# Performance work log

Measured on AMD Instinct MI355X. Metric: run time of the kernel, lower is better.

## Reference

```python
import jax, jax.numpy as jnp
import numpy as np
from jax import lax

B, EMB, CIN, COUT, K, H, W = 16, 768, 64, 64, 3, 112, 112
HID = EMB // 4  # reduction_ratio=4
TOTAL = COUT * CIN * K * K


def setup_inputs() -> dict:
    key = jax.random.key(0)
    k1, k2, k3, k4 = jax.random.split(key, 4)
    cls_token = jax.random.normal(k1, (B, 1, EMB), dtype=jnp.float32)
    features = jax.random.normal(k2, (B, CIN, H, W), dtype=jnp.float32)
    W1 = jax.random.normal(k3, (EMB, HID), dtype=jnp.float32) * 0.02
    b1 = jnp.zeros((HID,), dtype=jnp.float32)
    W2 = jax.random.normal(k4, (HID, TOTAL), dtype=jnp.float32) * 0.01
    b2 = jnp.zeros((TOTAL,), dtype=jnp.float32)
    return {"cls_token": cls_token, "features": features,
            "W1": W1, "b1": b1, "W2": W2, "b2": b2}


def _per_sample_conv(feat, kern):
    # feat: (CIN, H, W); kern: (COUT, CIN, K, K) -> (COUT, H, W)
    out = lax.conv_general_dilated(
        feat[None], kern, window_strides=(1, 1), padding="SAME",
        dimension_numbers=("NCHW", "OIHW", "NCHW"))
    return out[0]


def reference(cls_token, features, W1, b1, W2, b2):
    # Dynamic kernel generation from CLS token
    x = cls_token[:, 0, :]                      # (B, EMB)
    h = jax.nn.relu(x @ W1 + b1)                # (B, HID)
    params = jnp.tanh(h @ W2 + b2)              # (B, TOTAL)
    kernel = params.reshape(B, COUT, CIN, K, K)
    # Per-sample convolution (equivalent to unfold + bmm in torch)
    conv_feat = jax.vmap(_per_sample_conv)(features, kernel)  # (B, COUT, H, W)
    # in_channels == out_channels -> identity shortcut
    return conv_feat + features
```

## Files before the change

### kernel.cpp

```cpp
#include <hip/hip_runtime.h>
#include <hip/hip_bf16.h>

#define BB   16
#define EMB  768
#define CIN  64
#define COUT 64
#define HH   112
#define WW   112
#define HID  192
#define TOTAL 36864
#define KSZ  576
#define PW   114
#define CELLB 64
#define LROWB (PW * CELLB)
#define NCH  (4 * PW * 4)

typedef short bf16x8 __attribute__((ext_vector_type(8)));
typedef float f32x4  __attribute__((ext_vector_type(4)));
typedef int   i32x4  __attribute__((ext_vector_type(4)));

static __device__ __forceinline__ unsigned short f2bf(float f) {
    unsigned u = __float_as_uint(f);
    u += 0x7FFF + ((u >> 16) & 1);
    return (unsigned short)(u >> 16);
}

static __device__ __forceinline__ bf16x8 pack8(const float* v) {
    bf16x8 r;
    #pragma unroll
    for (int j = 0; j < 8; ++j) r[j] = (short)f2bf(v[j]);
    return r;
}

#define GLOAD_LDS16(g, l) \
    __builtin_amdgcn_global_load_lds((const __attribute__((address_space(1))) void*)(g), \
                                     (__attribute__((address_space(3))) void*)(l), 16, 0, 0)

__global__ __launch_bounds__(256) void mlp1_kernel(const float* __restrict__ cls,
                                                   const float* __restrict__ W1,
                                                   const float* __restrict__ b1,
                                                   float* __restrict__ h) {
    __shared__ float xs[EMB];
    __shared__ float red[16][17];
    const int b   = blockIdx.x / 12;
    const int jg  = blockIdx.x - 12 * b;
    const int tid = threadIdx.x;
    for (int i = tid; i < EMB; i += 256) xs[i] = cls[b * EMB + i];
    __syncthreads();
    const int j16 = tid & 15;
    const int kq  = tid >> 4;
    const int j   = jg * 16 + j16;
    float acc = 0.f;
    #pragma unroll
    for (int k = kq * 48; k < kq * 48 + 48; ++k) acc += xs[k] * W1[k * HID + j];
    red[j16][kq] = acc;
    __syncthreads();
    if (tid < 16) {
        float s = b1[jg * 16 + tid];
        #pragma unroll
        for (int q = 0; q < 16; ++q) s += red[tid][q];
        h[b * HID + jg * 16 + tid] = fmaxf(s, 0.f);
    }
}

__global__ __launch_bounds__(256) void pre_mlp2(const float* __restrict__ feat,
                                                unsigned short* __restrict__ P,
                                                const float* __restrict__ h,
                                                const float* __restrict__ W2,
                                                const float* __restrict__ b2,
                                                unsigned short* __restrict__ Ag) {
    __shared__ float hs[16 * 193];
    const int bid = blockIdx.x;
    const int tid = threadIdx.x;

    if (bid < HH * BB) {
        const int b = bid & 15;
        const int y = bid >> 4;
        if (tid < 16) {
            const int p    = tid >> 3;
            const int cell = ((tid >> 2) & 1) ? (PW - 1) : 0;
            const int sl   = tid & 3;
            char* Prow = (char*)P + ((size_t)(b * 2 + p) * PW + y + 1) * LROWB;
            *(i32x4*)(Prow + cell * CELLB + sl * 16) = (i32x4){0, 0, 0, 0};
        }
        const int o  = tid >> 5;
        const int p  = o >> 2;
        const int oo = o & 3;
        const int q  = tid & 31;
        if (q < 28) {
            const float* fb = feat + (((size_t)b * CIN + o * 8) * HH + y) * WW + 4 * q;
            unsigned short* Prow = P + ((size_t)(b * 2 + p) * PW + y + 1) * (PW * 32);
            f32x4 v[8];
            #pragma unroll
            for (int j = 0; j < 8; ++j) v[j] = *(const f32x4*)(fb + (size_t)j * (HH * WW));
            #pragma unroll
            for (int i = 0; i < 4; ++i) {
                unsigned short w[8];
                #pragma unroll
                for (int j = 0; j < 8; ++j) w[j] = f2bf(v[j][i]);
                *(bf16x8*)(Prow + (size_t)(4 * q + i + 1) * 32 + oo * 8) = *(bf16x8*)w;
            }
        }
    } else if (bid < HH * BB + 32) {
        const int idx = bid - HH * BB;
        const int b   = idx & 15;
        const int py  = (idx >> 4) ? (PW - 1) : 0;
        #pragma unroll
        for (int k = 0; k < 4; ++k) {
            const int i = tid + 256 * k;
            if (i < 912) {
                const int p = i / 456, j = i - p * 456;
                char* Prow = (char*)P + ((size_t)(b * 2 + p) * PW + py) * LROWB;
                ((i32x4*)Prow)[j] = (i32x4){0, 0, 0, 0};
            }
        }
    } else {
        const int blk = bid - (HH * BB + 32);
        for (int i = tid; i < BB * HID; i += 256) {
            const int bb = i / HID;
            hs[bb * 193 + (i - bb * HID)] = h[i];
        }
        __syncthreads();
        const int wave = tid >> 6;
        const int lane = tid & 63;
        const int lg   = lane >> 4;
        const int ln   = lane & 15;
        const int t0   = (blk * 4 + wave) * 16;

        bf16x8 a6[6];
        #pragma unroll
        for (int kk = 0; kk < 6; ++kk) {
            float v[8];
            #pragma unroll
            for (int j = 0; j < 8; ++j) v[j] = hs[ln * 193 + kk * 32 + lg * 8 + j];
            a6[kk] = pack8(v);
        }

        f32x4 acc = (f32x4){0.f, 0.f, 0.f, 0.f};
        #pragma unroll
        for (int kk = 0; kk < 6; ++kk) {
            float w[8];
            #pragma unroll
            for (int j = 0; j < 8; ++j)
                w[j] = W2[(size_t)(kk * 32 + lg * 8 + j) * TOTAL + t0 + ln];
            acc = __builtin_amdgcn_mfma_f32_16x16x32_bf16(a6[kk], pack8(w), acc, 0, 0, 0);
        }

        const int t    = t0 + ln;
        const float bias = b2[t];
        const int co  = t / KSZ;
        const int rem = t - co * KSZ;
        const int ci  = rem / 9;
        const int p9  = rem - ci * 9;
        const float idv = (p9 == 4 && co == ci) ? 1.f : 0.f;
        unsigned short* pA = Ag + (size_t)(p9 * 64 + co) * 64 + ci;
        #pragma unroll
        for (int rg = 0; rg < 4; ++rg) {
            const int bi = lg * 4 + rg;
            pA[(size_t)bi * TOTAL] = f2bf(tanhf(acc[rg] + bias) + idv);
        }
    }
}

__global__ __launch_bounds__(128, 2) void conv_kernel(const unsigned short* __restrict__ Ag,
                                                      const unsigned short* __restrict__ P,
                                                      float* __restrict__ out) {
    __shared__ __align__(16) char lds[4 * LROWB];
    const int tid = threadIdx.x;
    const int bid   = (blockIdx.x & 7) * 112 + (blockIdx.x >> 3);
    const int b     = bid / 56;
    const int strip = bid - b * 56;
    const int y0    = strip * 2;

    const int r    = tid >> 6;
    const int lane = tid & 63;
    const int lg   = lane >> 4;
    const int ln   = lane & 15;

    const unsigned short* Ab = Ag + (size_t)b * 9 * 4096;

    f32x4 acc[4][7];
    #pragma unroll
    for (int ct = 0; ct < 4; ++ct)
        #pragma unroll
        for (int t = 0; t < 7; ++t) acc[ct][t] = (f32x4){0.f, 0.f, 0.f, 0.f};

    #pragma unroll
    for (int h = 0; h < 2; ++h) {
        if (h) __syncthreads();
        const char* Pb = (const char*)P + ((size_t)(b * 2 + h) * PW + y0) * LROWB;
        #pragma unroll
        for (int k = 0; k < 15; ++k) {
            const int i = k * 128 + tid;
            if (i < NCH) {
                const int s    = i / (PW * 4);
                const int rem  = i - s * (PW * 4);
                const int cell = rem >> 2;
                const int sl   = rem & 3;
                const int g    = sl ^ (cell & 3);
                GLOAD_LDS16(Pb + (size_t)s * LROWB + cell * CELLB + g * 16,
                            lds + (size_t)i * 16);
            }
        }
        asm volatile("s_waitcnt vmcnt(0)" ::: "memory");
        __builtin_amdgcn_s_barrier();
        __builtin_amdgcn_sched_barrier(0);

        #pragma unroll
        for (int p9 = 0; p9 < 9; ++p9) {
            const int kh = p9 / 3, kw = p9 - 3 * kh;
            bf16x8 af[4];
            #pragma unroll
            for (int ct = 0; ct < 4; ++ct)
                af[ct] = *(const bf16x8*)(Ab + (size_t)(p9 * 64 + ct * 16 + ln) * 64
                                          + h * 32 + lg * 8);
            const char* lbase = lds + (r + kh) * LROWB;
            #pragma unroll
            for (int t = 0; t < 7; ++t) {
                const int cell = ln + kw + 16 * t;
                const int sl   = lg ^ (cell & 3);
                const bf16x8 bf = *(const bf16x8*)(lbase + cell * CELLB + sl * 16);
                #pragma unroll
                for (int ct = 0; ct < 4; ++ct)
                    acc[ct][t] = __builtin_amdgcn_mfma_f32_16x16x32_bf16(af[ct], bf, acc[ct][t], 0, 0, 0);
            }
        }
    }

    const int y = y0 + r;
    float* ob = out + (((size_t)b * COUT + lg * 4) * HH + y) * WW + ln;
    #pragma unroll
    for (int ct = 0; ct < 4; ++ct)
        #pragma unroll
        for (int t = 0; t < 7; ++t)
            #pragma unroll
            for (int rg = 0; rg < 4; ++rg)
                ob[((size_t)(ct * 16 + rg)) * HH * WW + t * 16] = acc[ct][t][rg];
}

extern "C" void kernel_launch(void* const* d_in, const int* in_sizes, int n_in,
                              void* d_out, int out_size, void* d_ws, size_t ws_size,
                              hipStream_t stream) {
    const float* cls      = (const float*)d_in[0];
    const float* features = (const float*)d_in[1];
    const float* W1       = (const float*)d_in[2];
    const float* b1       = (const float*)d_in[3];
    const float* W2       = (const float*)d_in[4];
    const float* b2       = (const float*)d_in[5];
    float* out = (float*)d_out;

    float*          h  = (float*)d_ws;
    unsigned short* Ag = (unsigned short*)(h + BB * HID);
    unsigned short* P  = Ag + (size_t)BB * 9 * 4096;

    mlp1_kernel<<<192, 256, 0, stream>>>(cls, W1, b1, h);
    pre_mlp2<<<HH * BB + 32 + 576, 256, 0, stream>>>(features, P, h, W2, b2, Ag);
    conv_kernel<<<896, 128, 0, stream>>>(Ag, P, out);
}
```

Baseline: 67.40 us.

## Pack all 64 channels per padded cell and load whole tile once

The padded bf16 feature buffer changes from two 32-channel halves to one 64-channel-per-cell layout (128-byte cells) with an 8-way XOR swizzle. The conv kernel now stages all four input rows with all channels into LDS in a single pass, removing the second load phase and its intermediate barrier. LDS use per block doubles, which may reduce the number of resident blocks per CU. The pre-pass block-to-row mapping is also rearranged.

```diff
diff --git a/kernel.cpp b/kernel.cpp
--- a/kernel.cpp
+++ b/kernel.cpp
@@ -11,9 +11,8 @@
 #define TOTAL 36864
 #define KSZ  576
 #define PW   114
-#define CELLB 64
-#define LROWB (PW * CELLB)
-#define NCH  (4 * PW * 4)
+#define CELL 128
+#define ROWB (PW * CELL)
 
 typedef short bf16x8 __attribute__((ext_vector_type(8)));
 typedef float f32x4  __attribute__((ext_vector_type(4)));
@@ -74,45 +73,37 @@
     const int tid = threadIdx.x;
 
     if (bid < HH * BB) {
-        const int b = bid & 15;
-        const int y = bid >> 4;
+        const int j = bid >> 3;
+        const int b = (bid & 7) * 2 + (j >= 112 ? 1 : 0);
+        const int y = j - (j >= 112 ? 112 : 0);
+        unsigned short* Prow = P + ((size_t)b * PW + y + 1) * (PW * 64);
         if (tid < 16) {
-            const int p    = tid >> 3;
-            const int cell = ((tid >> 2) & 1) ? (PW - 1) : 0;
-            const int sl   = tid & 3;
-            char* Prow = (char*)P + ((size_t)(b * 2 + p) * PW + y + 1) * LROWB;
-            *(i32x4*)(Prow + cell * CELLB + sl * 16) = (i32x4){0, 0, 0, 0};
-        }
-        const int o  = tid >> 5;
-        const int p  = o >> 2;
-        const int oo = o & 3;
-        const int q  = tid & 31;
+            const int cell = (tid >> 3) ? (PW - 1) : 0;
+            *(i32x4*)((char*)Prow + cell * CELL + (tid & 7) * 16) = (i32x4){0, 0, 0, 0};
+        }
+        const int o = tid >> 5;
+        const int q = tid & 31;
         if (q < 28) {
             const float* fb = feat + (((size_t)b * CIN + o * 8) * HH + y) * WW + 4 * q;
-            unsigned short* Prow = P + ((size_t)(b * 2 + p) * PW + y + 1) * (PW * 32);
             f32x4 v[8];
             #pragma unroll
-            for (int j = 0; j < 8; ++j) v[j] = *(const f32x4*)(fb + (size_t)j * (HH * WW));
+            for (int j2 = 0; j2 < 8; ++j2) v[j2] = *(const f32x4*)(fb + (size_t)j2 * (HH * WW));
             #pragma unroll
             for (int i = 0; i < 4; ++i) {
                 unsigned short w[8];
                 #pragma unroll
-                for (int j = 0; j < 8; ++j) w[j] = f2bf(v[j][i]);
-                *(bf16x8*)(Prow + (size_t)(4 * q + i + 1) * 32 + oo * 8) = *(bf16x8*)w;
+                for (int j2 = 0; j2 < 8; ++j2) w[j2] = f2bf(v[j2][i]);
+                *(bf16x8*)(Prow + (size_t)(4 * q + i + 1) * 64 + o * 8) = *(bf16x8*)w;
             }
         }
     } else if (bid < HH * BB + 32) {
         const int idx = bid - HH * BB;
         const int b   = idx & 15;
-        const int py  = (idx >> 4) ? (PW - 1) : 0;
+        unsigned short* Prow = P + ((size_t)b * PW + ((idx >> 4) ? (PW - 1) : 0)) * (PW * 64);
         #pragma unroll
         for (int k = 0; k < 4; ++k) {
             const int i = tid + 256 * k;
-            if (i < 912) {
-                const int p = i / 456, j = i - p * 456;
-                char* Prow = (char*)P + ((size_t)(b * 2 + p) * PW + py) * LROWB;
-                ((i32x4*)Prow)[j] = (i32x4){0, 0, 0, 0};
-            }
+            if (i < 912) ((i32x4*)Prow)[i] = (i32x4){0, 0, 0, 0};
         }
     } else {
         const int blk = bid - (HH * BB + 32);
@@ -165,7 +156,7 @@
 __global__ __launch_bounds__(128, 2) void conv_kernel(const unsigned short* __restrict__ Ag,
                                                       const unsigned short* __restrict__ P,
                                                       float* __restrict__ out) {
-    __shared__ __align__(16) char lds[4 * LROWB];
+    __shared__ __align__(16) char lds[4 * ROWB];
     const int tid = threadIdx.x;
     const int bid   = (blockIdx.x & 7) * 112 + (blockIdx.x >> 3);
     const int b     = bid / 56;
@@ -177,6 +168,24 @@
     const int lg   = lane >> 4;
     const int ln   = lane & 15;
 
+    const char* Pb = (const char*)P + ((size_t)b * PW + y0) * ROWB;
+    #pragma unroll
+    for (int k = 0; k < 28; ++k) {
+        const int i = k * 128 + tid;
+        const int s = i / 912;
+        const int jj = i - s * 912;
+        const int c = jj >> 3, g = jj & 7;
+        GLOAD_LDS16(Pb + (size_t)s * ROWB + c * CELL + ((g ^ (c & 7)) << 4),
+                    lds + (size_t)i * 16);
+    }
+    if (tid < 64) {
+        const int i = 3584 + tid;
+        const int jj = i - 3 * 912;
+        const int c = jj >> 3, g = jj & 7;
+        GLOAD_LDS16(Pb + (size_t)3 * ROWB + c * CELL + ((g ^ (c & 7)) << 4),
+                    lds + (size_t)i * 16);
+    }
+
     const unsigned short* Ab = Ag + (size_t)b * 9 * 4096;
 
     f32x4 acc[4][7];
@@ -185,27 +194,12 @@
         #pragma unroll
         for (int t = 0; t < 7; ++t) acc[ct][t] = (f32x4){0.f, 0.f, 0.f, 0.f};
 
-    #pragma unroll
-    for (int h = 0; h < 2; ++h) {
-        if (h) __syncthreads();
-        const char* Pb = (const char*)P + ((size_t)(b * 2 + h) * PW + y0) * LROWB;
-        #pragma unroll
-        for (int k = 0; k < 15; ++k) {
-            const int i = k * 128 + tid;
-            if (i < NCH) {
-                const int s    = i / (PW * 4);
-                const int rem  = i - s * (PW * 4);
-                const int cell = rem >> 2;
-                const int sl   = rem & 3;
-                const int g    = sl ^ (cell & 3);
-                GLOAD_LDS16(Pb + (size_t)s * LROWB + cell * CELLB + g * 16,
-                            lds + (size_t)i * 16);
-            }
-        }
-        asm volatile("s_waitcnt vmcnt(0)" ::: "memory");
-        __builtin_amdgcn_s_barrier();
-        __builtin_amdgcn_sched_barrier(0);
-
+    asm volatile("s_waitcnt vmcnt(0)" ::: "memory");
+    __builtin_amdgcn_s_barrier();
+    __builtin_amdgcn_sched_barrier(0);
+
+    #pragma unroll
+    for (int cib = 0; cib < 2; ++cib) {
         #pragma unroll
         for (int p9 = 0; p9 < 9; ++p9) {
             const int kh = p9 / 3, kw = p9 - 3 * kh;
@@ -213,13 +207,12 @@
             #pragma unroll
             for (int ct = 0; ct < 4; ++ct)
                 af[ct] = *(const bf16x8*)(Ab + (size_t)(p9 * 64 + ct * 16 + ln) * 64
-                                          + h * 32 + lg * 8);
-            const char* lbase = lds + (r + kh) * LROWB;
+                                          + cib * 32 + lg * 8);
+            const char* lbase = lds + (r + kh) * ROWB + (ln + kw) * CELL;
+            const int   sw    = (((cib * 4 + lg) ^ ((ln + kw) & 7)) << 4);
             #pragma unroll
             for (int t = 0; t < 7; ++t) {
-                const int cell = ln + kw + 16 * t;
-                const int sl   = lg ^ (cell & 3);
-                const bf16x8 bf = *(const bf16x8*)(lbase + cell * CELLB + sl * 16);
+                const bf16x8 bf = *(const bf16x8*)(lbase + t * (16 * CELL) + sw);
                 #pragma unroll
                 for (int ct = 0; ct < 4; ++ct)
                     acc[ct][t] = __builtin_amdgcn_mfma_f32_16x16x32_bf16(af[ct], bf, acc[ct][t], 0, 0, 0);
```

New measurement: 62.90 us. 1.07x faster.
